# Kernel tuning notes

Measured on AMD Instinct MI355X. Metric: run time of the kernel, lower is better.

## Reference

```python
import jax, jax.numpy as jnp
import numpy as np

# S6Layer dims: d_model=256; internal d_state=max(8,16//2)=8; expand=max(1.5,2*0.75)=1.5 -> d_inner=384
B, L, DM = 8, 4096, 256
DI, DS = 384, 8
CHUNK = 32  # seq_len > 64 path: chunked scan, state resets to 0 at every chunk (faithful to source)
EPS = 1e-5


def setup_inputs() -> dict:
    key = jax.random.key(0)
    ks = jax.random.split(key, 8)
    def w(k, shape, s=0.02):
        return jax.random.normal(k, shape, jnp.float32) * s
    return {
        "x": jax.random.normal(ks[0], (B, L, DM), jnp.float32),
        "gamma": jnp.ones((DM,), jnp.float32),
        "beta": jnp.zeros((DM,), jnp.float32),
        "W_in": w(ks[1], (3 * DI, DM)),
        "b_in": jnp.zeros((3 * DI,), jnp.float32),
        "W_dt": w(ks[2], (DI, DI)),
        "b_dt": jnp.zeros((DI,), jnp.float32),
        "A_log": jax.random.normal(ks[3], (DI, DS), jnp.float32),
        "D_vec": jax.random.normal(ks[4], (DI,), jnp.float32),
        "W_out": w(ks[5], (DM, DI)),
        "b_out": jnp.zeros((DM,), jnp.float32),
    }


def _layernorm(x, g, b):
    mu = jnp.mean(x, axis=-1, keepdims=True)
    var = jnp.mean(jnp.square(x - mu), axis=-1, keepdims=True)
    return (x - mu) * jax.lax.rsqrt(var + EPS) * g + b


def _chunked_scan(xp, dt, A):
    # xp, dt: [B, L, DI]; A: [DI, DS]. Each CHUNK-length block scans from h=0
    # (the torch code never propagates h across chunks for seq_len > 64).
    C = L // CHUNK
    xr = xp.reshape(B, C, CHUNK, DI)
    dtr = dt.reshape(B, C, CHUNK, DI)
    dA = jnp.exp(dtr[..., None] * A)              # [B, C, T, DI, DS]
    dA_t = jnp.moveaxis(dA, 2, 0)                 # [T, B, C, DI, DS]
    x_t = jnp.moveaxis(xr, 2, 0)                  # [T, B, C, DI]

    def step(h, inp):
        dA_i, x_i = inp
        h = h * dA_i + x_i[..., None]             # broadcast x over DS
        return h, jnp.sum(h, axis=-1)             # y_i: [B, C, DI]

    h0 = jnp.zeros((B, C, DI, DS), xp.dtype)
    _, ys = jax.lax.scan(step, h0, (dA_t, x_t))   # ys: [T, B, C, DI]
    return jnp.moveaxis(ys, 0, 2).reshape(B, L, DI)


def reference(x, gamma, beta, W_in, b_in, W_dt, b_dt, A_log, D_vec, W_out, b_out):
    residual = x
    xn = _layernorm(x, gamma, beta)
    xz = xn @ W_in.T + b_in                       # [B, L, 3*DI]
    x_proj, z, dt_in = jnp.split(xz, 3, axis=-1)
    x_proj = jax.nn.silu(x_proj)
    z = jax.nn.silu(z)
    dt = jax.nn.softplus(dt_in @ W_dt.T + b_dt)   # [B, L, DI]
    A = -jnp.exp(A_log)                           # [DI, DS]
    y = _chunked_scan(x_proj, dt, A)
    y = y * z + x_proj * D_vec
    return y @ W_out.T + b_out + residual
```

## Files before the change

### kernel.cpp

```cpp
#include <hip/hip_runtime.h>
#include <stdint.h>

#define B_  8
#define L_  4096
#define DM  256
#define DI  384
#define DS  8
#define M_  (B_*L_)

typedef float f32x4 __attribute__((ext_vector_type(4)));
typedef short s16x8 __attribute__((ext_vector_type(8)));

#define AS1(p) ((__attribute__((address_space(1))) void*)(p))
#define AS3(p) ((__attribute__((address_space(3))) void*)(p))

__device__ __forceinline__ unsigned short f2bf(float f) {
  union { float f; uint32_t u; } v; v.f = f;
  uint32_t r = v.u + 0x7FFFu + ((v.u >> 16) & 1u);
  return (unsigned short)(r >> 16);
}
__device__ __forceinline__ float bf2f(unsigned short h) {
  union { uint32_t u; float f; } v; v.u = ((uint32_t)h) << 16;
  return v.f;
}
__device__ __forceinline__ float silu_f(float x) {
  return x * __builtin_amdgcn_rcpf(1.f + __expf(-x));
}

__global__ __launch_bounds__(256) void cvt_kernel(
    const float* __restrict__ w0, const float* __restrict__ w1, const float* __restrict__ w2,
    unsigned short* __restrict__ o0, unsigned short* __restrict__ o1, unsigned short* __restrict__ o2) {
  int i = blockIdx.x * 256 + threadIdx.x;
  if (i < 3*DI*DM) o0[i] = f2bf(w0[i]);
  if (i < DI*DI)   o1[i] = f2bf(w1[i]);
  if (i < DM*DI)   o2[i] = f2bf(w2[i]);
}

__global__ __launch_bounds__(256) void ln_kernel(
    const float* __restrict__ x, const float* __restrict__ gamma, const float* __restrict__ beta,
    unsigned short* __restrict__ xn) {
  int token = blockIdx.x * 4 + (threadIdx.x >> 6);
  int lane  = threadIdx.x & 63;
  const float4 v = *(const float4*)(x + (size_t)token*DM + lane*4);
  float s  = v.x + v.y + v.z + v.w;
  float ss = v.x*v.x + v.y*v.y + v.z*v.z + v.w*v.w;
  #pragma unroll
  for (int off = 32; off > 0; off >>= 1) {
    s  += __shfl_xor(s,  off, 64);
    ss += __shfl_xor(ss, off, 64);
  }
  float mean = s * (1.f/DM);
  float var  = ss * (1.f/DM) - mean*mean;
  float rstd = rsqrtf(var + 1e-5f);
  const float4 g = *(const float4*)(gamma + lane*4);
  const float4 b = *(const float4*)(beta  + lane*4);
  ushort4 o;
  o.x = f2bf((v.x - mean)*rstd*g.x + b.x);
  o.y = f2bf((v.y - mean)*rstd*g.y + b.y);
  o.z = f2bf((v.z - mean)*rstd*g.z + b.z);
  o.w = f2bf((v.w - mean)*rstd*g.w + b.w);
  *(ushort4*)(xn + (size_t)token*DM + lane*4) = o;
}

template<int EPI, int KSTEPS, int MT>
__global__ __launch_bounds__(256, 3) void gemm_ws(
    const unsigned short* __restrict__ A,
    const unsigned short* __restrict__ Bw,
    const float* __restrict__ bias,
    unsigned short* __restrict__ o_xp, unsigned short* __restrict__ o_z,
    unsigned short* __restrict__ o_dtin,
    unsigned short* __restrict__ o_bf,
    const float* __restrict__ resid, float* __restrict__ o_f)
{
  constexpr int K    = KSTEPS * 32;
  constexpr int CPR  = K / 8;
  __shared__ unsigned short sB[64*K];
  __shared__ unsigned short sC[(EPI == 3) ? 2 : 4*32*72];

  const int t    = threadIdx.x;
  const int lane = t & 63;
  const int w    = t >> 6;
  const int fr   = lane & 15;
  const int fq   = lane >> 4;
  const int wm   = w * 32;

  const int q    = blockIdx.y * 128 + blockIdx.x;
  const int bx2  = (q & 7) * 16 + ((q >> 3) & 15);
  const int by2  = q >> 7;
  const int mbase0 = bx2 * (128 * MT);
  const int nbase  = by2 * 64;

  #pragma unroll
  for (int i = 0; i < (64*CPR)/256; ++i) {
    int c   = i*256 + t;
    int row = c / CPR;
    int j   = c - row*CPR;
    int jp  = (j & ~7) | ((j & 7) ^ (row & 7));
    __builtin_amdgcn_global_load_lds(AS1(Bw + (size_t)(nbase + row)*K + jp*8),
                                     AS3(sB + c*8), 16, 0, 0);
  }

  const unsigned short* sBrE = sB + (size_t)fr*K + ( fq      ^ (fr & 7))*8;
  const unsigned short* sBrO = sB + (size_t)fr*K + ((fq | 4) ^ (fr & 7))*8;

  float bvv[4];
  #pragma unroll
  for (int ni = 0; ni < 4; ++ni) bvv[ni] = bias[nbase + ni*16 + fr];

  unsigned short* sCw = sC + w*(32*72);

  __syncthreads();

  #pragma unroll
  for (int mt = 0; mt < MT; ++mt) {
    const int mbase = mbase0 + mt*128;
    const unsigned short* gA0 = A + (size_t)(mbase + wm + fr)*K + fq*8;
    const unsigned short* gA1 = gA0 + (size_t)16*K;

    f32x4 acc[2][4];
    #pragma unroll
    for (int mi = 0; mi < 2; ++mi)
      #pragma unroll
      for (int ni = 0; ni < 4; ++ni) acc[mi][ni] = (f32x4){0.f, 0.f, 0.f, 0.f};

    #pragma unroll
    for (int kt = 0; kt < KSTEPS; ++kt) {
      s16x8 a0 = *(const s16x8*)(gA0 + kt*32);
      s16x8 a1 = *(const s16x8*)(gA1 + kt*32);
      const unsigned short* bb = (kt & 1) ? sBrO : sBrE;
      s16x8 bfr[4];
      #pragma unroll
      for (int ni = 0; ni < 4; ++ni)
        bfr[ni] = *(const s16x8*)(bb + ni*16*K + (kt >> 1)*64);
      #pragma unroll
      for (int ni = 0; ni < 4; ++ni) {
        acc[0][ni] = __builtin_amdgcn_mfma_f32_16x16x32_bf16(a0, bfr[ni], acc[0][ni], 0, 0, 0);
        acc[1][ni] = __builtin_amdgcn_mfma_f32_16x16x32_bf16(a1, bfr[ni], acc[1][ni], 0, 0, 0);
      }
    }

    if constexpr (EPI == 3) {
      #pragma unroll
      for (int ni = 0; ni < 4; ++ni) {
        int gn = nbase + ni*16 + fr;
        #pragma unroll
        for (int mi = 0; mi < 2; ++mi) {
          int gm0 = mbase + wm + mi*16 + fq*4;
          #pragma unroll
          for (int r = 0; r < 4; ++r) {
            size_t gm = (size_t)(gm0 + r);
            o_f[gm*DM + gn] = acc[mi][ni][r] + bvv[ni] + resid[gm*DM + gn];
          }
        }
      }
    } else {
      const bool do_silu = (EPI == 1) && (by2 < 12);
      #pragma unroll
      for (int ni = 0; ni < 4; ++ni) {
        int cn = ni*16 + fr;
        #pragma unroll
        for (int mi = 0; mi < 2; ++mi) {
          int rm0 = mi*16 + fq*4;
          #pragma unroll
          for (int r = 0; r < 4; ++r) {
            float c = acc[mi][ni][r] + bvv[ni];
            if constexpr (EPI == 1) { if (do_silu) c = silu_f(c); }
            else                    { c = (c > 20.f) ? c : __logf(1.f + __expf(c)); }
            sCw[(rm0 + r)*72 + cn] = f2bf(c);
          }
        }
      }
      asm volatile("s_waitcnt lgkmcnt(0)" ::: "memory");
      unsigned short* dst;
      int colbase;
      if constexpr (EPI == 1) {
        dst = (by2 < 6) ? o_xp : (by2 < 12) ? o_z : o_dtin;
        colbase = (by2 % 6) * 64;
      } else {
        dst = o_bf; colbase = nbase;
      }
      const int rr = lane >> 3, cc = (lane & 7) * 8;
      #pragma unroll
      for (int it = 0; it < 4; ++it) {
        int row32 = rr + it*8;
        s16x8 v = *(const s16x8*)(sCw + row32*72 + cc);
        *(s16x8*)(dst + (size_t)(mbase + wm + row32)*DI + colbase + cc) = v;
      }
    }
  }
}

__global__ __launch_bounds__(384) void scan_kernel(
    const unsigned short* __restrict__ xp, const unsigned short* __restrict__ dt,
    const unsigned short* __restrict__ zb, const float* __restrict__ A_log,
    const float* __restrict__ D_vec, unsigned short* __restrict__ yz) {
  int g  = blockIdx.x;
  int di = threadIdx.x;
  size_t base = (size_t)g * 32 * DI + di;
  float a[DS];
  #pragma unroll
  for (int s = 0; s < DS; ++s) a[s] = -__expf(A_log[di*DS + s]);
  float Dv = D_vec[di];
  float h[DS] = {0.f,0.f,0.f,0.f,0.f,0.f,0.f,0.f};
  for (int tt = 0; tt < 32; ++tt) {
    size_t idx = base + (size_t)tt * DI;
    float xv  = bf2f(xp[idx]);
    float dtv = bf2f(dt[idx]);
    float y = 0.f;
    #pragma unroll
    for (int s = 0; s < DS; ++s) {
      h[s] = h[s] * __expf(dtv * a[s]) + xv;
      y += h[s];
    }
    float zv = bf2f(zb[idx]);
    yz[idx] = f2bf(y * zv + xv * Dv);
  }
}

extern "C" void kernel_launch(void* const* d_in, const int* in_sizes, int n_in,
                              void* d_out, int out_size, void* d_ws, size_t ws_size,
                              hipStream_t stream) {
  const float* x     = (const float*)d_in[0];
  const float* gamma = (const float*)d_in[1];
  const float* beta  = (const float*)d_in[2];
  const float* W_in  = (const float*)d_in[3];
  const float* b_in  = (const float*)d_in[4];
  const float* W_dt  = (const float*)d_in[5];
  const float* b_dt  = (const float*)d_in[6];
  const float* A_log = (const float*)d_in[7];
  const float* D_vec = (const float*)d_in[8];
  const float* W_out = (const float*)d_in[9];
  const float* b_out = (const float*)d_in[10];
  float* out = (float*)d_out;

  char* ws = (char*)d_ws;
  size_t off = 0;
  auto alloc = [&](size_t bytes) -> char* {
    char* p = ws + off; off += (bytes + 255) & ~(size_t)255; return p;
  };
  unsigned short* xn    = (unsigned short*)alloc((size_t)M_*DM*2);
  unsigned short* xpb   = (unsigned short*)alloc((size_t)M_*DI*2);
  unsigned short* zb    = (unsigned short*)alloc((size_t)M_*DI*2);
  unsigned short* dtin  = (unsigned short*)alloc((size_t)M_*DI*2);
  unsigned short* dtb   = (unsigned short*)alloc((size_t)M_*DI*2);
  unsigned short* yzb   = dtin;
  unsigned short* winb  = (unsigned short*)alloc((size_t)3*DI*DM*2);
  unsigned short* wdtb  = (unsigned short*)alloc((size_t)DI*DI*2);
  unsigned short* woutb = (unsigned short*)alloc((size_t)DM*DI*2);

  cvt_kernel<<<dim3((3*DI*DM + 255)/256), 256, 0, stream>>>(W_in, W_dt, W_out, winb, wdtb, woutb);
  ln_kernel<<<dim3(M_/4), 256, 0, stream>>>(x, gamma, beta, xn);
  gemm_ws<1, 8, 2><<<dim3(128, (3*DI)/64), 256, 0, stream>>>(
      xn, winb, b_in, xpb, zb, dtin, nullptr, nullptr, nullptr);
  gemm_ws<2, 12, 2><<<dim3(128, DI/64), 256, 0, stream>>>(
      dtin, wdtb, b_dt, nullptr, nullptr, nullptr, dtb, nullptr, nullptr);
  scan_kernel<<<dim3(M_/32), DI, 0, stream>>>(xpb, dtb, zb, A_log, D_vec, yzb);
  gemm_ws<3, 12, 2><<<dim3(128, DM/64), 256, 0, stream>>>(
      yzb, woutb, b_out, nullptr, nullptr, nullptr, nullptr, x, out);
}
```

Baseline: 224.2 us.

## Fuse dt GEMM, chunked scan and output GEMM into one per-tile kernel

Replaces three launches (dt projection GEMM, selective scan, output projection GEMM) with one kernel that handles 64 tokens per block. The block keeps the softplus(dt) tile and then the y*z+x*D result in a swizzled 48KB LDS buffer, so the dt and yz intermediates never make a round trip through global memory. Costs: MFMA operands come straight from global without LDS staging, the large LDS footprint limits occupancy, and each thread runs the scan serially over 3 channel slots.

```diff
diff --git a/kernel.cpp b/kernel.cpp
--- a/kernel.cpp
+++ b/kernel.cpp
@@ -190,30 +190,122 @@
   }
 }
 
-__global__ __launch_bounds__(384) void scan_kernel(
-    const unsigned short* __restrict__ xp, const unsigned short* __restrict__ dt,
-    const unsigned short* __restrict__ zb, const float* __restrict__ A_log,
-    const float* __restrict__ D_vec, unsigned short* __restrict__ yz) {
-  int g  = blockIdx.x;
-  int di = threadIdx.x;
-  size_t base = (size_t)g * 32 * DI + di;
-  float a[DS];
-  #pragma unroll
-  for (int s = 0; s < DS; ++s) a[s] = -__expf(A_log[di*DS + s]);
-  float Dv = D_vec[di];
-  float h[DS] = {0.f,0.f,0.f,0.f,0.f,0.f,0.f,0.f};
-  for (int tt = 0; tt < 32; ++tt) {
-    size_t idx = base + (size_t)tt * DI;
-    float xv  = bf2f(xp[idx]);
-    float dtv = bf2f(dt[idx]);
-    float y = 0.f;
-    #pragma unroll
-    for (int s = 0; s < DS; ++s) {
-      h[s] = h[s] * __expf(dtv * a[s]) + xv;
-      y += h[s];
-    }
-    float zv = bf2f(zb[idx]);
-    yz[idx] = f2bf(y * zv + xv * Dv);
+__global__ __launch_bounds__(256, 2) void s6_tail(
+    const unsigned short* __restrict__ dtin,
+    const unsigned short* __restrict__ xp,
+    const unsigned short* __restrict__ zb,
+    const unsigned short* __restrict__ Wdt,
+    const unsigned short* __restrict__ Wout,
+    const float* __restrict__ b_dt, const float* __restrict__ b_out,
+    const float* __restrict__ A_log, const float* __restrict__ D_vec,
+    const float* __restrict__ resid, float* __restrict__ o_f)
+{
+  __shared__ unsigned short sDT[64*384];
+  const int t    = threadIdx.x;
+  const int lane = t & 63;
+  const int w    = t >> 6;
+  const int fr   = lane & 15;
+  const int fq   = lane >> 4;
+  const int wn16 = w * 16;
+  const int mbase = blockIdx.x * 64;
+
+  const unsigned short* gA = dtin + (size_t)(mbase + fr)*DI + fq*8;
+  #pragma unroll
+  for (int np = 0; np < 6; ++np) {
+    const unsigned short* gB = Wdt + (size_t)(np*64 + wn16 + fr)*DI + fq*8;
+    float bv = b_dt[np*64 + wn16 + fr];
+    f32x4 acc[4];
+    #pragma unroll
+    for (int mi = 0; mi < 4; ++mi) acc[mi] = (f32x4){0.f, 0.f, 0.f, 0.f};
+    #pragma unroll
+    for (int kt = 0; kt < 12; ++kt) {
+      s16x8 bfrg = *(const s16x8*)(gB + kt*32);
+      #pragma unroll
+      for (int mi = 0; mi < 4; ++mi) {
+        s16x8 afrg = *(const s16x8*)(gA + mi*16*DI + kt*32);
+        acc[mi] = __builtin_amdgcn_mfma_f32_16x16x32_bf16(afrg, bfrg, acc[mi], 0, 0, 0);
+      }
+    }
+    #pragma unroll
+    for (int mi = 0; mi < 4; ++mi)
+      #pragma unroll
+      for (int r = 0; r < 4; ++r) {
+        int row = mi*16 + fq*4 + r;
+        int cn  = np*64 + wn16 + fr;
+        float c = acc[mi][r] + bv;
+        c = (c > 20.f) ? c : __logf(1.f + __expf(c));
+        int j  = cn >> 3;
+        int jp = (j & ~7) | ((j & 7) ^ (row & 7));
+        sDT[row*DI + jp*8 + (cn & 7)] = f2bf(c);
+      }
+  }
+  __syncthreads();
+
+  {
+    int   chunk[3], di[3], jb[3], del[3];
+    float av[3][8], hs[3][8], Dv[3];
+    const unsigned short *gx[3], *gz[3];
+    #pragma unroll
+    for (int i = 0; i < 3; ++i) {
+      int u    = t + i*256;
+      chunk[i] = (u >= 384) ? 1 : 0;
+      di[i]    = u - chunk[i]*384;
+      jb[i]    = di[i] >> 3;
+      del[i]   = di[i] & 7;
+      #pragma unroll
+      for (int s = 0; s < DS; ++s) { av[i][s] = -__expf(A_log[di[i]*DS + s]); hs[i][s] = 0.f; }
+      Dv[i] = D_vec[di[i]];
+      gx[i] = xp + (size_t)(mbase + chunk[i]*32)*DI + di[i];
+      gz[i] = zb + (size_t)(mbase + chunk[i]*32)*DI + di[i];
+    }
+    for (int tt = 0; tt < 32; ++tt) {
+      #pragma unroll
+      for (int i = 0; i < 3; ++i) {
+        int tok  = chunk[i]*32 + tt;
+        int jp   = (jb[i] & ~7) | ((jb[i] & 7) ^ (tok & 7));
+        int sidx = tok*DI + jp*8 + del[i];
+        float dtv = bf2f(sDT[sidx]);
+        float xv  = bf2f(gx[i][(size_t)tt*DI]);
+        float y = 0.f;
+        #pragma unroll
+        for (int s = 0; s < DS; ++s) {
+          hs[i][s] = hs[i][s]*__expf(dtv*av[i][s]) + xv;
+          y += hs[i][s];
+        }
+        float zv = bf2f(gz[i][(size_t)tt*DI]);
+        sDT[sidx] = f2bf(y*zv + xv*Dv[i]);
+      }
+    }
+  }
+  __syncthreads();
+
+  const int lbE = ( fq      ^ (fr & 7))*8;
+  const int lbO = ((fq | 4) ^ (fr & 7))*8;
+  #pragma unroll
+  for (int np = 0; np < 4; ++np) {
+    const unsigned short* gB = Wout + (size_t)(np*64 + wn16 + fr)*DI + fq*8;
+    float bv = b_out[np*64 + wn16 + fr];
+    f32x4 acc[4];
+    #pragma unroll
+    for (int mi = 0; mi < 4; ++mi) acc[mi] = (f32x4){0.f, 0.f, 0.f, 0.f};
+    #pragma unroll
+    for (int kt = 0; kt < 12; ++kt) {
+      s16x8 bfrg = *(const s16x8*)(gB + kt*32);
+      int off = ((kt & 1) ? lbO : lbE) + (kt >> 1)*64;
+      #pragma unroll
+      for (int mi = 0; mi < 4; ++mi) {
+        s16x8 afrg = *(const s16x8*)(sDT + (mi*16 + fr)*DI + off);
+        acc[mi] = __builtin_amdgcn_mfma_f32_16x16x32_bf16(afrg, bfrg, acc[mi], 0, 0, 0);
+      }
+    }
+    #pragma unroll
+    for (int mi = 0; mi < 4; ++mi)
+      #pragma unroll
+      for (int r = 0; r < 4; ++r) {
+        size_t gm = (size_t)(mbase + mi*16 + fq*4 + r);
+        int gn = np*64 + wn16 + fr;
+        o_f[gm*DM + gn] = acc[mi][r] + bv + resid[gm*DM + gn];
+      }
   }
 }
 
@@ -242,8 +334,6 @@
   unsigned short* xpb   = (unsigned short*)alloc((size_t)M_*DI*2);
   unsigned short* zb    = (unsigned short*)alloc((size_t)M_*DI*2);
   unsigned short* dtin  = (unsigned short*)alloc((size_t)M_*DI*2);
-  unsigned short* dtb   = (unsigned short*)alloc((size_t)M_*DI*2);
-  unsigned short* yzb   = dtin;
   unsigned short* winb  = (unsigned short*)alloc((size_t)3*DI*DM*2);
   unsigned short* wdtb  = (unsigned short*)alloc((size_t)DI*DI*2);
   unsigned short* woutb = (unsigned short*)alloc((size_t)DM*DI*2);
@@ -252,9 +342,6 @@
   ln_kernel<<<dim3(M_/4), 256, 0, stream>>>(x, gamma, beta, xn);
   gemm_ws<1, 8, 2><<<dim3(128, (3*DI)/64), 256, 0, stream>>>(
       xn, winb, b_in, xpb, zb, dtin, nullptr, nullptr, nullptr);
-  gemm_ws<2, 12, 2><<<dim3(128, DI/64), 256, 0, stream>>>(
-      dtin, wdtb, b_dt, nullptr, nullptr, nullptr, dtb, nullptr, nullptr);
-  scan_kernel<<<dim3(M_/32), DI, 0, stream>>>(xpb, dtb, zb, A_log, D_vec, yzb);
-  gemm_ws<3, 12, 2><<<dim3(128, DM/64), 256, 0, stream>>>(
-      yzb, woutb, b_out, nullptr, nullptr, nullptr, nullptr, x, out);
-}
+  s6_tail<<<dim3(M_/64), 256, 0, stream>>>(
+      dtin, xpb, zb, wdtb, woutb, b_dt, b_out, A_log, D_vec, x, out);
+}
```

After: 257.4 us. 14.8% more time.

## Give each GEMM wave a 64-row tile instead of looping two 32-row passes

Applied to the files above, without the earlier changes.

Each wave now computes a 64x64 output tile with a 4x4 grid of MFMA accumulators in a single K loop, replacing two sequential 128-row passes of 32 rows per wave. Every B fragment read from LDS now feeds four MFMAs instead of two, halving LDS reads per MFMA and removing the outer loop. The cost is twice the accumulator registers (64 floats per lane), which under the 3-blocks-per-CU launch bound may cause spills or lower occupancy. The bf16 epilogue is split into two 32-row halves so the LDS staging buffer keeps its size.

```diff
diff --git a/kernel.cpp b/kernel.cpp
--- a/kernel.cpp
+++ b/kernel.cpp
@@ -62,7 +62,7 @@
   *(ushort4*)(xn + (size_t)token*DM + lane*4) = o;
 }
 
-template<int EPI, int KSTEPS, int MT>
+template<int EPI, int KSTEPS>
 __global__ __launch_bounds__(256, 3) void gemm_ws(
     const unsigned short* __restrict__ A,
     const unsigned short* __restrict__ Bw,
@@ -82,13 +82,13 @@
   const int w    = t >> 6;
   const int fr   = lane & 15;
   const int fq   = lane >> 4;
-  const int wm   = w * 32;
+  const int wm   = w * 64;
 
   const int q    = blockIdx.y * 128 + blockIdx.x;
   const int bx2  = (q & 7) * 16 + ((q >> 3) & 15);
   const int by2  = q >> 7;
-  const int mbase0 = bx2 * (128 * MT);
-  const int nbase  = by2 * 64;
+  const int mbase = bx2 * 256;
+  const int nbase = by2 * 64;
 
   #pragma unroll
   for (int i = 0; i < (64*CPR)/256; ++i) {
@@ -111,59 +111,65 @@
 
   __syncthreads();
 
-  #pragma unroll
-  for (int mt = 0; mt < MT; ++mt) {
-    const int mbase = mbase0 + mt*128;
-    const unsigned short* gA0 = A + (size_t)(mbase + wm + fr)*K + fq*8;
-    const unsigned short* gA1 = gA0 + (size_t)16*K;
-
-    f32x4 acc[2][4];
-    #pragma unroll
-    for (int mi = 0; mi < 2; ++mi)
-      #pragma unroll
-      for (int ni = 0; ni < 4; ++ni) acc[mi][ni] = (f32x4){0.f, 0.f, 0.f, 0.f};
-
-    #pragma unroll
-    for (int kt = 0; kt < KSTEPS; ++kt) {
-      s16x8 a0 = *(const s16x8*)(gA0 + kt*32);
-      s16x8 a1 = *(const s16x8*)(gA1 + kt*32);
-      const unsigned short* bb = (kt & 1) ? sBrO : sBrE;
-      s16x8 bfr[4];
-      #pragma unroll
-      for (int ni = 0; ni < 4; ++ni)
-        bfr[ni] = *(const s16x8*)(bb + ni*16*K + (kt >> 1)*64);
-      #pragma unroll
-      for (int ni = 0; ni < 4; ++ni) {
-        acc[0][ni] = __builtin_amdgcn_mfma_f32_16x16x32_bf16(a0, bfr[ni], acc[0][ni], 0, 0, 0);
-        acc[1][ni] = __builtin_amdgcn_mfma_f32_16x16x32_bf16(a1, bfr[ni], acc[1][ni], 0, 0, 0);
-      }
-    }
-
-    if constexpr (EPI == 3) {
-      #pragma unroll
-      for (int ni = 0; ni < 4; ++ni) {
-        int gn = nbase + ni*16 + fr;
+  f32x4 acc[4][4];
+  #pragma unroll
+  for (int mi = 0; mi < 4; ++mi)
+    #pragma unroll
+    for (int ni = 0; ni < 4; ++ni) acc[mi][ni] = (f32x4){0.f, 0.f, 0.f, 0.f};
+
+  #pragma unroll
+  for (int kt = 0; kt < KSTEPS; ++kt) {
+    s16x8 af[4];
+    #pragma unroll
+    for (int mi = 0; mi < 4; ++mi)
+      af[mi] = *(const s16x8*)(A + (size_t)(mbase + wm + mi*16 + fr)*K + fq*8 + kt*32);
+    const unsigned short* bb = (kt & 1) ? sBrO : sBrE;
+    s16x8 bfr[4];
+    #pragma unroll
+    for (int ni = 0; ni < 4; ++ni)
+      bfr[ni] = *(const s16x8*)(bb + ni*16*K + (kt >> 1)*64);
+    #pragma unroll
+    for (int ni = 0; ni < 4; ++ni)
+      #pragma unroll
+      for (int mi = 0; mi < 4; ++mi)
+        acc[mi][ni] = __builtin_amdgcn_mfma_f32_16x16x32_bf16(af[mi], bfr[ni], acc[mi][ni], 0, 0, 0);
+  }
+
+  if constexpr (EPI == 3) {
+    #pragma unroll
+    for (int ni = 0; ni < 4; ++ni) {
+      int gn = nbase + ni*16 + fr;
+      #pragma unroll
+      for (int mi = 0; mi < 4; ++mi) {
+        int gm0 = mbase + wm + mi*16 + fq*4;
         #pragma unroll
-        for (int mi = 0; mi < 2; ++mi) {
-          int gm0 = mbase + wm + mi*16 + fq*4;
-          #pragma unroll
-          for (int r = 0; r < 4; ++r) {
-            size_t gm = (size_t)(gm0 + r);
-            o_f[gm*DM + gn] = acc[mi][ni][r] + bvv[ni] + resid[gm*DM + gn];
-          }
+        for (int r = 0; r < 4; ++r) {
+          size_t gm = (size_t)(gm0 + r);
+          o_f[gm*DM + gn] = acc[mi][ni][r] + bvv[ni] + resid[gm*DM + gn];
         }
       }
+    }
+  } else {
+    const bool do_silu = (EPI == 1) && (by2 < 12);
+    unsigned short* dst;
+    int colbase;
+    if constexpr (EPI == 1) {
+      dst = (by2 < 6) ? o_xp : (by2 < 12) ? o_z : o_dtin;
+      colbase = (by2 % 6) * 64;
     } else {
-      const bool do_silu = (EPI == 1) && (by2 < 12);
+      dst = o_bf; colbase = nbase;
+    }
+    #pragma unroll
+    for (int p = 0; p < 2; ++p) {
       #pragma unroll
       for (int ni = 0; ni < 4; ++ni) {
         int cn = ni*16 + fr;
         #pragma unroll
-        for (int mi = 0; mi < 2; ++mi) {
-          int rm0 = mi*16 + fq*4;
+        for (int mi2 = 0; mi2 < 2; ++mi2) {
+          int rm0 = mi2*16 + fq*4;
           #pragma unroll
           for (int r = 0; r < 4; ++r) {
-            float c = acc[mi][ni][r] + bvv[ni];
+            float c = acc[p*2 + mi2][ni][r] + bvv[ni];
             if constexpr (EPI == 1) { if (do_silu) c = silu_f(c); }
             else                    { c = (c > 20.f) ? c : __logf(1.f + __expf(c)); }
             sCw[(rm0 + r)*72 + cn] = f2bf(c);
@@ -171,20 +177,12 @@
         }
       }
       asm volatile("s_waitcnt lgkmcnt(0)" ::: "memory");
-      unsigned short* dst;
-      int colbase;
-      if constexpr (EPI == 1) {
-        dst = (by2 < 6) ? o_xp : (by2 < 12) ? o_z : o_dtin;
-        colbase = (by2 % 6) * 64;
-      } else {
-        dst = o_bf; colbase = nbase;
-      }
       const int rr = lane >> 3, cc = (lane & 7) * 8;
       #pragma unroll
       for (int it = 0; it < 4; ++it) {
         int row32 = rr + it*8;
         s16x8 v = *(const s16x8*)(sCw + row32*72 + cc);
-        *(s16x8*)(dst + (size_t)(mbase + wm + row32)*DI + colbase + cc) = v;
+        *(s16x8*)(dst + (size_t)(mbase + wm + p*32 + row32)*DI + colbase + cc) = v;
       }
     }
   }
@@ -250,11 +248,11 @@
 
   cvt_kernel<<<dim3((3*DI*DM + 255)/256), 256, 0, stream>>>(W_in, W_dt, W_out, winb, wdtb, woutb);
   ln_kernel<<<dim3(M_/4), 256, 0, stream>>>(x, gamma, beta, xn);
-  gemm_ws<1, 8, 2><<<dim3(128, (3*DI)/64), 256, 0, stream>>>(
+  gemm_ws<1, 8><<<dim3(128, (3*DI)/64), 256, 0, stream>>>(
       xn, winb, b_in, xpb, zb, dtin, nullptr, nullptr, nullptr);
-  gemm_ws<2, 12, 2><<<dim3(128, DI/64), 256, 0, stream>>>(
+  gemm_ws<2, 12><<<dim3(128, DI/64), 256, 0, stream>>>(
       dtin, wdtb, b_dt, nullptr, nullptr, nullptr, dtb, nullptr, nullptr);
   scan_kernel<<<dim3(M_/32), DI, 0, stream>>>(xpb, dtb, zb, A_log, D_vec, yzb);
-  gemm_ws<3, 12, 2><<<dim3(128, DM/64), 256, 0, stream>>>(
+  gemm_ws<3, 12><<<dim3(128, DM/64), 256, 0, stream>>>(
       yzb, woutb, b_out, nullptr, nullptr, nullptr, nullptr, x, out);
 }
```

New measurement: 224.5 us. About the same (+0.1%).

## Fold dt projection weights into input projection to remove second GEMM

Applied to the files above, without the earlier changes.

Precomputes W_dt·W_in[dt rows] and the combined bias in a new prep kernel, so the first GEMM yields dt_in@W_dt directly and applies softplus in its epilogue. This removes the separate dt GEMM launch and its round trip of an M×DI bf16 intermediate through memory. The scan now overwrites the dt buffer in place with y·z. The folded weight is computed per call by a naive 384-block kernel, which adds launch and compute cost. Rounding behaviour also shifts because the composed weight is quantised once to bf16 instead of the intermediate activation.

```diff
diff --git a/kernel.cpp b/kernel.cpp
--- a/kernel.cpp
+++ b/kernel.cpp
@@ -28,12 +28,36 @@
 }
 
 __global__ __launch_bounds__(256) void cvt_kernel(
-    const float* __restrict__ w0, const float* __restrict__ w1, const float* __restrict__ w2,
-    unsigned short* __restrict__ o0, unsigned short* __restrict__ o1, unsigned short* __restrict__ o2) {
+    const float* __restrict__ w0, const float* __restrict__ w2,
+    const float* __restrict__ b_in,
+    unsigned short* __restrict__ o0, unsigned short* __restrict__ o2,
+    float* __restrict__ biasc) {
   int i = blockIdx.x * 256 + threadIdx.x;
   if (i < 3*DI*DM) o0[i] = f2bf(w0[i]);
-  if (i < DI*DI)   o1[i] = f2bf(w1[i]);
   if (i < DM*DI)   o2[i] = f2bf(w2[i]);
+  if (i < 2*DI)    biasc[i] = b_in[i];
+}
+
+__global__ __launch_bounds__(256) void prep_kernel(
+    const float* __restrict__ W_in, const float* __restrict__ b_in,
+    const float* __restrict__ W_dt, const float* __restrict__ b_dt,
+    unsigned short* __restrict__ winb, float* __restrict__ biasc) {
+  int nb = blockIdx.x;
+  if (nb < DI) {
+    int c = threadIdx.x;
+    float acc = 0.f;
+    for (int k = 0; k < DI; ++k)
+      acc += W_dt[(size_t)nb*DI + k] * W_in[(size_t)(2*DI + k)*DM + c];
+    winb[(size_t)(2*DI + nb)*DM + c] = f2bf(acc);
+  } else {
+    int n = (nb - DI)*256 + threadIdx.x;
+    if (n < DI) {
+      float acc = b_dt[n];
+      for (int k = 0; k < DI; ++k)
+        acc += W_dt[(size_t)n*DI + k] * b_in[2*DI + k];
+      biasc[2*DI + n] = acc;
+    }
+  }
 }
 
 __global__ __launch_bounds__(256) void ln_kernel(
@@ -68,8 +92,7 @@
     const unsigned short* __restrict__ Bw,
     const float* __restrict__ bias,
     unsigned short* __restrict__ o_xp, unsigned short* __restrict__ o_z,
-    unsigned short* __restrict__ o_dtin,
-    unsigned short* __restrict__ o_bf,
+    unsigned short* __restrict__ o_dt,
     const float* __restrict__ resid, float* __restrict__ o_f)
 {
   constexpr int K    = KSTEPS * 32;
@@ -154,7 +177,7 @@
         }
       }
     } else {
-      const bool do_silu = (EPI == 1) && (by2 < 12);
+      const bool do_silu = (by2 < 12);
       #pragma unroll
       for (int ni = 0; ni < 4; ++ni) {
         int cn = ni*16 + fr;
@@ -164,21 +187,15 @@
           #pragma unroll
           for (int r = 0; r < 4; ++r) {
             float c = acc[mi][ni][r] + bvv[ni];
-            if constexpr (EPI == 1) { if (do_silu) c = silu_f(c); }
-            else                    { c = (c > 20.f) ? c : __logf(1.f + __expf(c)); }
+            c = do_silu ? silu_f(c)
+                        : ((c > 20.f) ? c : __logf(1.f + __expf(c)));
             sCw[(rm0 + r)*72 + cn] = f2bf(c);
           }
         }
       }
       asm volatile("s_waitcnt lgkmcnt(0)" ::: "memory");
-      unsigned short* dst;
-      int colbase;
-      if constexpr (EPI == 1) {
-        dst = (by2 < 6) ? o_xp : (by2 < 12) ? o_z : o_dtin;
-        colbase = (by2 % 6) * 64;
-      } else {
-        dst = o_bf; colbase = nbase;
-      }
+      unsigned short* dst = (by2 < 6) ? o_xp : (by2 < 12) ? o_z : o_dt;
+      int colbase = (by2 % 6) * 64;
       const int rr = lane >> 3, cc = (lane & 7) * 8;
       #pragma unroll
       for (int it = 0; it < 4; ++it) {
@@ -191,9 +208,9 @@
 }
 
 __global__ __launch_bounds__(384) void scan_kernel(
-    const unsigned short* __restrict__ xp, const unsigned short* __restrict__ dt,
+    const unsigned short* __restrict__ xp, unsigned short* dt_yz,
     const unsigned short* __restrict__ zb, const float* __restrict__ A_log,
-    const float* __restrict__ D_vec, unsigned short* __restrict__ yz) {
+    const float* __restrict__ D_vec) {
   int g  = blockIdx.x;
   int di = threadIdx.x;
   size_t base = (size_t)g * 32 * DI + di;
@@ -205,7 +222,7 @@
   for (int tt = 0; tt < 32; ++tt) {
     size_t idx = base + (size_t)tt * DI;
     float xv  = bf2f(xp[idx]);
-    float dtv = bf2f(dt[idx]);
+    float dtv = bf2f(dt_yz[idx]);
     float y = 0.f;
     #pragma unroll
     for (int s = 0; s < DS; ++s) {
@@ -213,7 +230,7 @@
       y += h[s];
     }
     float zv = bf2f(zb[idx]);
-    yz[idx] = f2bf(y * zv + xv * Dv);
+    dt_yz[idx] = f2bf(y * zv + xv * Dv);
   }
 }
 
@@ -241,20 +258,17 @@
   unsigned short* xn    = (unsigned short*)alloc((size_t)M_*DM*2);
   unsigned short* xpb   = (unsigned short*)alloc((size_t)M_*DI*2);
   unsigned short* zb    = (unsigned short*)alloc((size_t)M_*DI*2);
-  unsigned short* dtin  = (unsigned short*)alloc((size_t)M_*DI*2);
   unsigned short* dtb   = (unsigned short*)alloc((size_t)M_*DI*2);
-  unsigned short* yzb   = dtin;
   unsigned short* winb  = (unsigned short*)alloc((size_t)3*DI*DM*2);
-  unsigned short* wdtb  = (unsigned short*)alloc((size_t)DI*DI*2);
   unsigned short* woutb = (unsigned short*)alloc((size_t)DM*DI*2);
-
-  cvt_kernel<<<dim3((3*DI*DM + 255)/256), 256, 0, stream>>>(W_in, W_dt, W_out, winb, wdtb, woutb);
+  float*          biasc = (float*)alloc((size_t)3*DI*4);
+
+  cvt_kernel<<<dim3((3*DI*DM + 255)/256), 256, 0, stream>>>(W_in, W_out, b_in, winb, woutb, biasc);
+  prep_kernel<<<dim3(DI + 2), 256, 0, stream>>>(W_in, b_in, W_dt, b_dt, winb, biasc);
   ln_kernel<<<dim3(M_/4), 256, 0, stream>>>(x, gamma, beta, xn);
   gemm_ws<1, 8, 2><<<dim3(128, (3*DI)/64), 256, 0, stream>>>(
-      xn, winb, b_in, xpb, zb, dtin, nullptr, nullptr, nullptr);
-  gemm_ws<2, 12, 2><<<dim3(128, DI/64), 256, 0, stream>>>(
-      dtin, wdtb, b_dt, nullptr, nullptr, nullptr, dtb, nullptr, nullptr);
-  scan_kernel<<<dim3(M_/32), DI, 0, stream>>>(xpb, dtb, zb, A_log, D_vec, yzb);
+      xn, winb, biasc, xpb, zb, dtb, nullptr, nullptr);
+  scan_kernel<<<dim3(M_/32), DI, 0, stream>>>(xpb, dtb, zb, A_log, D_vec);
   gemm_ws<3, 12, 2><<<dim3(128, DM/64), 256, 0, stream>>>(
-      yzb, woutb, b_out, nullptr, nullptr, nullptr, nullptr, x, out);
-}
+      dtb, woutb, b_out, nullptr, nullptr, nullptr, x, out);
+}
```

After: 217.4 us. -3.0%, faster.
